# Performance work log

Hardware: AMD Instinct MI355X
Metric: run time of the kernel (lower is better)

Reference implementation:

```python
import jax, jax.numpy as jnp
import numpy as np

N_NODES = 100000
EPS_BN = 1e-5


def setup_inputs() -> dict:
    key = jax.random.key(0)
    k1, k2, k3, k4, k5, k6 = jax.random.split(key, 6)
    x = jax.random.normal(k1, (N_NODES, 200), dtype=jnp.float32)
    edge_index = jax.random.randint(k2, (2, 1600000), 0, N_NODES, dtype=jnp.int64)
    # GCNConv params (Glorot-ish scale)
    W = jax.random.normal(k3, (200, 64), dtype=jnp.float32) * (1.0 / np.sqrt(200.0))
    b = jax.random.normal(k4, (64,), dtype=jnp.float32) * 0.01
    # BatchNorm1d affine params
    bn_weight = jax.random.normal(k5, (64,), dtype=jnp.float32) * 0.1 + 1.0
    bn_bias = jax.random.normal(k6, (64,), dtype=jnp.float32) * 0.1
    return {"x": x, "edge_index": edge_index, "W": W, "b": b,
            "bn_weight": bn_weight, "bn_bias": bn_bias}


def _gcn_conv(x, edge_index, W, b):
    n = x.shape[0]
    # linear transform first (PyG GCNConv order): [N, 64]
    xw = x @ W
    # add self-loops
    loop = jnp.arange(n, dtype=edge_index.dtype)
    src = jnp.concatenate([edge_index[0], loop])
    dst = jnp.concatenate([edge_index[1], loop])
    # symmetric normalization: deg over dst (incl. self loops)
    deg = jax.ops.segment_sum(jnp.ones_like(dst, dtype=xw.dtype), dst, num_segments=n)
    dinv = jnp.where(deg > 0, jax.lax.rsqrt(deg), 0.0)
    norm = dinv[src] * dinv[dst]  # [E+N]
    # gather-scale-scatter: out[dst] += norm * xw[src]
    msg = xw[src] * norm[:, None]
    out = jax.ops.segment_sum(msg, dst, num_segments=n)
    return out + b


def reference(x, edge_index, W, b, bn_weight, bn_bias):
    h = _gcn_conv(x, edge_index, W, b)
    h = jax.nn.relu(h)
    # BatchNorm1d in training mode: biased batch statistics over nodes
    mean = jnp.mean(h, axis=0)
    var = jnp.mean(jnp.square(h - mean), axis=0)
    y = (h - mean) * jax.lax.rsqrt(var + EPS_BN) * bn_weight + bn_bias
    return y
```

## Files before the change

kernel.cpp:

```cpp
#include <hip/hip_runtime.h>

#define N_NODES 100000
#define N_EDGES 1600000
#define K_DIM   200
#define C_DIM   64
#define EPS_BN  1e-5f
#define MT      128
#define NKB     25
#define SLICE_U ((size_t)N_NODES * 16)
#define NPX     12500
#define MAXD    48

typedef int      vi4 __attribute__((ext_vector_type(4)));
typedef float    vf4 __attribute__((ext_vector_type(4)));
typedef unsigned vu4 __attribute__((ext_vector_type(4)));

__device__ __forceinline__ ushort f2bf(float f) {
    unsigned u = __float_as_uint(f);
    u = (u + 0x7FFFu + ((u >> 16) & 1u)) >> 16;
    return (ushort)u;
}

__global__ __launch_bounds__(256) void k_fillslot(
        const int* __restrict__ src, const int* __restrict__ dst,
        int* __restrict__ cursor, int* __restrict__ slot) {
    unsigned lo = (blockIdx.x & 7) * NPX;
    int i0 = (blockIdx.x >> 3) * 256 + threadIdx.x;
    int stride = (gridDim.x >> 3) * 256;
    for (int i = i0; i < N_EDGES / 4; i += stride) {
        vi4 d = __builtin_nontemporal_load((const vi4*)dst + i);
        bool mx = (unsigned)(d.x - lo) < NPX;
        bool my = (unsigned)(d.y - lo) < NPX;
        bool mz = (unsigned)(d.z - lo) < NPX;
        bool mw = (unsigned)(d.w - lo) < NPX;
        if (mx | my | mz | mw) {
            vi4 s = __builtin_nontemporal_load((const vi4*)src + i);
            if (mx) { int p = atomicAdd(&cursor[d.x], 1); if (p < MAXD) slot[(size_t)p * N_NODES + d.x] = s.x; }
            if (my) { int p = atomicAdd(&cursor[d.y], 1); if (p < MAXD) slot[(size_t)p * N_NODES + d.y] = s.y; }
            if (mz) { int p = atomicAdd(&cursor[d.z], 1); if (p < MAXD) slot[(size_t)p * N_NODES + d.z] = s.z; }
            if (mw) { int p = atomicAdd(&cursor[d.w], 1); if (p < MAXD) slot[(size_t)p * N_NODES + d.w] = s.w; }
        }
    }
}

__global__ __launch_bounds__(256) void k_gemm2(const float* __restrict__ x,
                                               const float* __restrict__ W,
                                               const int* __restrict__ cursor,
                                               ushort* __restrict__ xsp) {
    __shared__ float xT[8][MT];
    __shared__ float Wt[8][C_DIM];
    int tid = threadIdx.x;
    int tx = tid & 15;
    int ty = tid >> 4;
    int row0 = blockIdx.x * MT;

    int lrow = tid >> 1;
    int lk   = (tid & 1) * 4;
    int grow = row0 + lrow;
    if (grow > N_NODES - 1) grow = N_NODES - 1;
    const float* xp = x + (size_t)grow * K_DIM + lk;
    int wk = tid >> 4;
    int wc = (tid & 15) * 4;

    float acc[8][4];
    #pragma unroll
    for (int i = 0; i < 8; ++i)
        #pragma unroll
        for (int j = 0; j < 4; ++j) acc[i][j] = 0.f;

    float4 xr = *(const float4*)xp;
    float4 wr = {0,0,0,0};
    if (tid < 128) wr = *(const float4*)(W + wk * C_DIM + wc);

    for (int kb = 0; kb < NKB; ++kb) {
        xT[lk + 0][lrow] = xr.x;
        xT[lk + 1][lrow] = xr.y;
        xT[lk + 2][lrow] = xr.z;
        xT[lk + 3][lrow] = xr.w;
        if (tid < 128) *(float4*)&Wt[wk][wc] = wr;
        __syncthreads();
        if (kb < NKB - 1) {
            xr = *(const float4*)(xp + (kb + 1) * 8);
            if (tid < 128) wr = *(const float4*)(W + ((kb + 1) * 8 + wk) * C_DIM + wc);
        }
        #pragma unroll
        for (int k = 0; k < 8; ++k) {
            float4 xa = *(const float4*)&xT[k][ty * 8];
            float4 xb = *(const float4*)&xT[k][ty * 8 + 4];
            float4 wv = *(const float4*)&Wt[k][tx * 4];
            float xv[8] = {xa.x, xa.y, xa.z, xa.w, xb.x, xb.y, xb.z, xb.w};
            #pragma unroll
            for (int i = 0; i < 8; ++i) {
                acc[i][0] = fmaf(xv[i], wv.x, acc[i][0]);
                acc[i][1] = fmaf(xv[i], wv.y, acc[i][1]);
                acc[i][2] = fmaf(xv[i], wv.z, acc[i][2]);
                acc[i][3] = fmaf(xv[i], wv.w, acc[i][3]);
            }
        }
        __syncthreads();
    }
    int sl  = tx >> 2;
    int pos = (tx & 3) * 4;
    #pragma unroll
    for (int i = 0; i < 8; ++i) {
        int r = row0 + ty * 8 + i;
        if (r < N_NODES) {
            float dv = rsqrtf((float)cursor[r] + 1.0f);
            ushort4 o = {f2bf(acc[i][0] * dv), f2bf(acc[i][1] * dv),
                         f2bf(acc[i][2] * dv), f2bf(acc[i][3] * dv)};
            *(ushort4*)(xsp + (size_t)sl * SLICE_U + (size_t)r * 16 + pos) = o;
        }
    }
}

#define UNPK0(u, k) { acc[k] = __uint_as_float((u) << 16); \
                      acc[k+1] = __uint_as_float((u) & 0xFFFF0000u); }
#define UNPKA(u, k) { acc[k] += __uint_as_float((u) << 16); \
                      acc[k+1] += __uint_as_float((u) & 0xFFFF0000u); }

__global__ __launch_bounds__(256) void k_gath4(
        const int* __restrict__ slot, const int* __restrict__ cursor,
        const ushort* __restrict__ xsp, const float* __restrict__ b,
        ushort* __restrict__ hp2, float* __restrict__ stats) {
    int tid  = threadIdx.x;
    int lane = tid & 63;
    int widx = tid >> 6;
    int bid  = blockIdx.x;
    int slice = (bid & 7) >> 1;
    int chunk = ((bid >> 3) * 2 + (bid & 1)) * 4 + widx;
    int nchunks = (gridDim.x >> 3) * 8;
    const ushort* xs = xsp + (size_t)slice * SLICE_U;
    const float*  bs = b + slice * 16;
    float s1[16], s2[16];
    #pragma unroll
    for (int i = 0; i < 16; ++i) { s1[i] = 0.f; s2[i] = 0.f; }

    for (int n0 = chunk * 64; n0 < N_NODES; n0 += nchunks * 64) {
        int n = n0 + lane;
        bool act = n < N_NODES;
        int dg = 0;
        float dn = 0.f;
        float acc[16];
        if (act) {
            dg = __builtin_nontemporal_load(cursor + n);
            dn = rsqrtf((float)dg + 1.0f);
            if (dg > MAXD) dg = MAXD;
            const uint4* rp = (const uint4*)(xs + (size_t)n * 16);
            uint4 a = rp[0], c = rp[1];
            UNPK0(a.x, 0)  UNPK0(a.y, 2)  UNPK0(a.z, 4)  UNPK0(a.w, 6)
            UNPK0(c.x, 8)  UNPK0(c.y, 10) UNPK0(c.z, 12) UNPK0(c.w, 14)
        } else {
            #pragma unroll
            for (int i = 0; i < 16; ++i) acc[i] = 0.f;
        }
        const int* sp = slot + n;
        int p = 0;
        for (; p + 2 <= dg; p += 2) {
            int s0  = sp[(size_t)p * N_NODES];
            int s1e = sp[(size_t)(p + 1) * N_NODES];
            const uint4* p0 = (const uint4*)(xs + (size_t)s0 * 16);
            const uint4* p1 = (const uint4*)(xs + (size_t)s1e * 16);
            uint4 a0 = p0[0], c0 = p0[1];
            uint4 a1 = p1[0], c1 = p1[1];
            UNPKA(a0.x, 0)  UNPKA(a0.y, 2)  UNPKA(a0.z, 4)  UNPKA(a0.w, 6)
            UNPKA(c0.x, 8)  UNPKA(c0.y, 10) UNPKA(c0.z, 12) UNPKA(c0.w, 14)
            UNPKA(a1.x, 0)  UNPKA(a1.y, 2)  UNPKA(a1.z, 4)  UNPKA(a1.w, 6)
            UNPKA(c1.x, 8)  UNPKA(c1.y, 10) UNPKA(c1.z, 12) UNPKA(c1.w, 14)
        }
        if (p < dg) {
            int s0 = sp[(size_t)p * N_NODES];
            const uint4* p0 = (const uint4*)(xs + (size_t)s0 * 16);
            uint4 a0 = p0[0], c0 = p0[1];
            UNPKA(a0.x, 0)  UNPKA(a0.y, 2)  UNPKA(a0.z, 4)  UNPKA(a0.w, 6)
            UNPKA(c0.x, 8)  UNPKA(c0.y, 10) UNPKA(c0.z, 12) UNPKA(c0.w, 14)
        }
        if (act) {
            unsigned pk[8];
            #pragma unroll
            for (int i2 = 0; i2 < 8; ++i2) {
                float lo = fmaxf(fmaf(dn, acc[2*i2+0], bs[2*i2+0]), 0.f);
                float hi = fmaxf(fmaf(dn, acc[2*i2+1], bs[2*i2+1]), 0.f);
                s1[2*i2+0] += lo; s2[2*i2+0] = fmaf(lo, lo, s2[2*i2+0]);
                s1[2*i2+1] += hi; s2[2*i2+1] = fmaf(hi, hi, s2[2*i2+1]);
                pk[i2] = (unsigned)f2bf(lo) | ((unsigned)f2bf(hi) << 16);
            }
            vu4 w0 = {pk[0], pk[1], pk[2], pk[3]};
            vu4 w1 = {pk[4], pk[5], pk[6], pk[7]};
            ushort* hb = hp2 + ((size_t)slice * N_NODES + (size_t)n) * 16;
            __builtin_nontemporal_store(w0, (vu4*)hb);
            __builtin_nontemporal_store(w1, (vu4*)(hb + 8));
        }
    }

    __shared__ float red[4][32];
    #pragma unroll
    for (int i = 0; i < 16; ++i) {
        float a = s1[i], c = s2[i];
        #pragma unroll
        for (int m = 1; m <= 32; m <<= 1) {
            a += __shfl_xor(a, m);
            c += __shfl_xor(c, m);
        }
        if (lane == 0) { red[widx][i] = a; red[widx][16 + i] = c; }
    }
    __syncthreads();
    if (tid < 32) {
        float v = red[0][tid] + red[1][tid] + red[2][tid] + red[3][tid];
        int ch = slice * 16 + (tid & 15);
        unsafeAtomicAdd(&stats[(tid >> 4) * 64 + ch], v);
    }
}

__global__ __launch_bounds__(256) void k_final_p(
        const ushort* __restrict__ hp2, const float* __restrict__ stats,
        const float* __restrict__ bnw, const float* __restrict__ bnb,
        float* __restrict__ out) {
    int tid = blockIdx.x * 256 + threadIdx.x;
    if (tid >= N_NODES * 8) return;
    int half = tid & 7;
    int n    = tid >> 3;
    int slice = half >> 1, sub = half & 1;
    int cb = slice * 16 + sub * 8;
    float sc[8], sh[8];
    #pragma unroll
    for (int j = 0; j < 8; ++j) {
        int c = cb + j;
        float mean = stats[c] * (1.0f / N_NODES);
        float var  = stats[64 + c] * (1.0f / N_NODES) - mean * mean;
        float s = rsqrtf(var + EPS_BN) * bnw[c];
        sc[j] = s;
        sh[j] = bnb[c] - mean * s;
    }
    vu4 v = __builtin_nontemporal_load(
        (const vu4*)(hp2 + ((size_t)slice * N_NODES + (size_t)n) * 16 + sub * 8));
    vf4 h0, h1;
    h0.x = __uint_as_float(v.x << 16); h0.y = __uint_as_float(v.x & 0xFFFF0000u);
    h0.z = __uint_as_float(v.y << 16); h0.w = __uint_as_float(v.y & 0xFFFF0000u);
    h1.x = __uint_as_float(v.z << 16); h1.y = __uint_as_float(v.z & 0xFFFF0000u);
    h1.z = __uint_as_float(v.w << 16); h1.w = __uint_as_float(v.w & 0xFFFF0000u);
    vf4 o0, o1;
    o0.x = fmaf(h0.x, sc[0], sh[0]); o0.y = fmaf(h0.y, sc[1], sh[1]);
    o0.z = fmaf(h0.z, sc[2], sh[2]); o0.w = fmaf(h0.w, sc[3], sh[3]);
    o1.x = fmaf(h1.x, sc[4], sh[4]); o1.y = fmaf(h1.y, sc[5], sh[5]);
    o1.z = fmaf(h1.z, sc[6], sh[6]); o1.w = fmaf(h1.w, sc[7], sh[7]);
    float* op = out + (size_t)n * C_DIM + cb;
    __builtin_nontemporal_store(o0, (vf4*)op);
    __builtin_nontemporal_store(o1, (vf4*)(op + 4));
}

extern "C" void kernel_launch(void* const* d_in, const int* in_sizes, int n_in,
                              void* d_out, int out_size, void* d_ws, size_t ws_size,
                              hipStream_t stream) {
    const float* x   = (const float*)d_in[0];
    const int*   ei  = (const int*)d_in[1];
    const float* W   = (const float*)d_in[2];
    const float* b   = (const float*)d_in[3];
    const float* bnw = (const float*)d_in[4];
    const float* bnb = (const float*)d_in[5];
    float* out = (float*)d_out;

    const int* src = ei;
    const int* dst = ei + N_EDGES;
    char* ws = (char*)d_ws;

    const size_t SZ_I = 400128;
    const size_t OFF_STAT = SZ_I;
    const size_t OFF_SLOT = SZ_I + 512;
    const size_t OFF_H    = OFF_SLOT + (size_t)N_NODES * MAXD * 4;
    const size_t ZERO_B   = SZ_I + 512;

    ushort* xsp = (ushort*)out;
    const int GEMM_GRID = (N_NODES + MT - 1) / MT;

    int*    cursor = (int*)ws;
    float*  stats  = (float*)(ws + OFF_STAT);
    int*    slot   = (int*)(ws + OFF_SLOT);
    ushort* hp2    = (ushort*)(ws + OFF_H);

    hipMemsetAsync(d_ws, 0, ZERO_B, stream);

    k_fillslot <<<2048, 256, 0, stream>>>(src, dst, cursor, slot);
    k_gemm2    <<<GEMM_GRID, 256, 0, stream>>>(x, W, cursor, xsp);
    k_gath4    <<<1568, 256, 0, stream>>>(slot, cursor, xsp, b, hp2, stats);
    k_final_p  <<<(N_NODES * 8 + 255) / 256, 256, 0, stream>>>(hp2, stats, bnw, bnb, out);
    (void)ws_size;
}
```

Measured before the change: 201.1 us.

## Unroll gather loop by four, double gather grid, load src unconditionally in fill

The neighbor gather loop now handles four neighbors per iteration before falling back to pairs and singles, so more independent row loads are in flight per thread. The gather kernel launch is doubled to 3136 blocks, which raises parallelism but changes how chunks map to blocks. The slot-fill kernel now reads src and dst with ordinary loads and always loads src instead of only when a dst falls in its partition. That removes a branch but adds src traffic for edges the block ignores. The wider unroll also raises register pressure.

```diff
diff --git a/kernel.cpp b/kernel.cpp
--- a/kernel.cpp
+++ b/kernel.cpp
@@ -28,18 +28,16 @@
     int i0 = (blockIdx.x >> 3) * 256 + threadIdx.x;
     int stride = (gridDim.x >> 3) * 256;
     for (int i = i0; i < N_EDGES / 4; i += stride) {
-        vi4 d = __builtin_nontemporal_load((const vi4*)dst + i);
+        vi4 d = ((const vi4*)dst)[i];
+        vi4 s = ((const vi4*)src)[i];
         bool mx = (unsigned)(d.x - lo) < NPX;
         bool my = (unsigned)(d.y - lo) < NPX;
         bool mz = (unsigned)(d.z - lo) < NPX;
         bool mw = (unsigned)(d.w - lo) < NPX;
-        if (mx | my | mz | mw) {
-            vi4 s = __builtin_nontemporal_load((const vi4*)src + i);
-            if (mx) { int p = atomicAdd(&cursor[d.x], 1); if (p < MAXD) slot[(size_t)p * N_NODES + d.x] = s.x; }
-            if (my) { int p = atomicAdd(&cursor[d.y], 1); if (p < MAXD) slot[(size_t)p * N_NODES + d.y] = s.y; }
-            if (mz) { int p = atomicAdd(&cursor[d.z], 1); if (p < MAXD) slot[(size_t)p * N_NODES + d.z] = s.z; }
-            if (mw) { int p = atomicAdd(&cursor[d.w], 1); if (p < MAXD) slot[(size_t)p * N_NODES + d.w] = s.w; }
-        }
+        if (mx) { int p = atomicAdd(&cursor[d.x], 1); if (p < MAXD) slot[(size_t)p * N_NODES + d.x] = s.x; }
+        if (my) { int p = atomicAdd(&cursor[d.y], 1); if (p < MAXD) slot[(size_t)p * N_NODES + d.y] = s.y; }
+        if (mz) { int p = atomicAdd(&cursor[d.z], 1); if (p < MAXD) slot[(size_t)p * N_NODES + d.z] = s.z; }
+        if (mw) { int p = atomicAdd(&cursor[d.w], 1); if (p < MAXD) slot[(size_t)p * N_NODES + d.w] = s.w; }
     }
 }
 
@@ -117,6 +115,8 @@
                       acc[k+1] = __uint_as_float((u) & 0xFFFF0000u); }
 #define UNPKA(u, k) { acc[k] += __uint_as_float((u) << 16); \
                       acc[k+1] += __uint_as_float((u) & 0xFFFF0000u); }
+#define ROWACC(aa, cc) { UNPKA(aa.x, 0)  UNPKA(aa.y, 2)  UNPKA(aa.z, 4)  UNPKA(aa.w, 6) \
+                         UNPKA(cc.x, 8)  UNPKA(cc.y, 10) UNPKA(cc.z, 12) UNPKA(cc.w, 14) }
 
 __global__ __launch_bounds__(256) void k_gath4(
         const int* __restrict__ slot, const int* __restrict__ cursor,
@@ -155,24 +155,35 @@
         }
         const int* sp = slot + n;
         int p = 0;
+        for (; p + 4 <= dg; p += 4) {
+            int e0 = sp[(size_t)(p + 0) * N_NODES];
+            int e1 = sp[(size_t)(p + 1) * N_NODES];
+            int e2 = sp[(size_t)(p + 2) * N_NODES];
+            int e3 = sp[(size_t)(p + 3) * N_NODES];
+            const uint4* q0 = (const uint4*)(xs + (size_t)e0 * 16);
+            const uint4* q1 = (const uint4*)(xs + (size_t)e1 * 16);
+            const uint4* q2 = (const uint4*)(xs + (size_t)e2 * 16);
+            const uint4* q3 = (const uint4*)(xs + (size_t)e3 * 16);
+            uint4 a0 = q0[0], c0 = q0[1];
+            uint4 a1 = q1[0], c1 = q1[1];
+            uint4 a2 = q2[0], c2 = q2[1];
+            uint4 a3 = q3[0], c3 = q3[1];
+            ROWACC(a0, c0)  ROWACC(a1, c1)  ROWACC(a2, c2)  ROWACC(a3, c3)
+        }
         for (; p + 2 <= dg; p += 2) {
-            int s0  = sp[(size_t)p * N_NODES];
-            int s1e = sp[(size_t)(p + 1) * N_NODES];
-            const uint4* p0 = (const uint4*)(xs + (size_t)s0 * 16);
-            const uint4* p1 = (const uint4*)(xs + (size_t)s1e * 16);
-            uint4 a0 = p0[0], c0 = p0[1];
-            uint4 a1 = p1[0], c1 = p1[1];
-            UNPKA(a0.x, 0)  UNPKA(a0.y, 2)  UNPKA(a0.z, 4)  UNPKA(a0.w, 6)
-            UNPKA(c0.x, 8)  UNPKA(c0.y, 10) UNPKA(c0.z, 12) UNPKA(c0.w, 14)
-            UNPKA(a1.x, 0)  UNPKA(a1.y, 2)  UNPKA(a1.z, 4)  UNPKA(a1.w, 6)
-            UNPKA(c1.x, 8)  UNPKA(c1.y, 10) UNPKA(c1.z, 12) UNPKA(c1.w, 14)
+            int e0 = sp[(size_t)(p + 0) * N_NODES];
+            int e1 = sp[(size_t)(p + 1) * N_NODES];
+            const uint4* q0 = (const uint4*)(xs + (size_t)e0 * 16);
+            const uint4* q1 = (const uint4*)(xs + (size_t)e1 * 16);
+            uint4 a0 = q0[0], c0 = q0[1];
+            uint4 a1 = q1[0], c1 = q1[1];
+            ROWACC(a0, c0)  ROWACC(a1, c1)
         }
         if (p < dg) {
-            int s0 = sp[(size_t)p * N_NODES];
-            const uint4* p0 = (const uint4*)(xs + (size_t)s0 * 16);
-            uint4 a0 = p0[0], c0 = p0[1];
-            UNPKA(a0.x, 0)  UNPKA(a0.y, 2)  UNPKA(a0.z, 4)  UNPKA(a0.w, 6)
-            UNPKA(c0.x, 8)  UNPKA(c0.y, 10) UNPKA(c0.z, 12) UNPKA(c0.w, 14)
+            int e0 = sp[(size_t)p * N_NODES];
+            const uint4* q0 = (const uint4*)(xs + (size_t)e0 * 16);
+            uint4 a0 = q0[0], c0 = q0[1];
+            ROWACC(a0, c0)
         }
         if (act) {
             unsigned pk[8];
@@ -281,7 +292,7 @@
 
     k_fillslot <<<2048, 256, 0, stream>>>(src, dst, cursor, slot);
     k_gemm2    <<<GEMM_GRID, 256, 0, stream>>>(x, W, cursor, xsp);
-    k_gath4    <<<1568, 256, 0, stream>>>(slot, cursor, xsp, b, hp2, stats);
+    k_gath4    <<<3136, 256, 0, stream>>>(slot, cursor, xsp, b, hp2, stats);
     k_final_p  <<<(N_NODES * 8 + 255) / 256, 256, 0, stream>>>(hp2, stats, bnw, bnb, out);
     (void)ws_size;
 }
```

Measured after the change: 201.3 us (median of 2 runs). Within noise of the previous version (+0.1%).
